# Optimization experiments

Measured on AMD Instinct MI355X. Metric: run time of the kernel, lower is better.

The kernel has to match this reference:

```python
import jax, jax.numpy as jnp
import numpy as np

KAPPA = 5  # kNN neighbors per node (module hardcodes kappas = [5]*B, topk of KAPPA+2)


def build_graph(inputs):
    """Vectorized equivalent of get_graph(): returns flat (src, dst, edge_weight)
    over the B*S node space. Filtered kNN edges (dst < 2) are masked via weight 0,
    which is mathematically identical to removing them (gcn_norm uses edge weights)."""
    B, S, _ = inputs.shape
    diff = inputs[:, :, None, :] - inputs[:, None, :, :]            # [B,S,S,2]
    deltas = jnp.sqrt(jnp.sum(diff * diff, axis=-1))                # torch.cdist
    eye = jnp.eye(S, dtype=bool)
    d = jnp.where(eye[None], jnp.inf, deltas)                       # fill_diagonal_(inf)
    nodes = jnp.arange(2, S, dtype=jnp.int32)                       # non-depot nodes
    # depot edges: 0 -> i  and  i -> 1  for i in [2, S)
    src_dep = jnp.concatenate([jnp.zeros(S - 2, jnp.int32), nodes])
    dst_dep = jnp.concatenate([nodes, jnp.ones(S - 2, jnp.int32)])
    # kNN edges: 7 nearest per non-depot node (diag=inf so i never selected)
    _, idx = jax.lax.top_k(-d[:, 2:, :], KAPPA + 2)                 # [B, S-2, 7]
    src_knn = jnp.broadcast_to(nodes[:, None], (S - 2, KAPPA + 2)).reshape(-1)
    dst_knn = idx.reshape(B, -1).astype(jnp.int32)                  # [B, 7*(S-2)]
    mask_knn = (dst_knn >= 2).astype(jnp.float32)                   # drop depot dsts
    src = jnp.concatenate([jnp.broadcast_to(src_dep[None], (B, src_dep.shape[0])), jnp.broadcast_to(src_knn[None], (B, src_knn.shape[0]))], axis=1)
    dst = jnp.concatenate([jnp.broadcast_to(dst_dep[None], (B, dst_dep.shape[0])), dst_knn], axis=1)
    ew = jnp.concatenate([jnp.ones((B, dst_dep.shape[0]), jnp.float32), mask_knn], axis=1)
    offs = (jnp.arange(B, dtype=jnp.int32) * S)[:, None]            # batch node offset
    return (src + offs).reshape(-1), (dst + offs).reshape(-1), ew.reshape(-1)


def gcn_conv(x, src, dst, norm, self_norm, W, b, N):
    h = x @ W                                                       # GCNConv linear
    agg = jax.ops.segment_sum(h[src] * norm[:, None], dst, num_segments=N)
    agg = agg + h * self_norm[:, None]                              # self-loop term
    return agg + b


def gnn_forward(x, src, dst, ew, W0, b0, W1, b1, W2, b2):
    N = x.shape[0]
    deg = jax.ops.segment_sum(ew, dst, num_segments=N) + 1.0        # +1 self-loop
    dinv = 1.0 / jnp.sqrt(deg)
    norm = dinv[src] * dinv[dst] * ew                               # sym gcn_norm
    self_norm = dinv * dinv
    h = jax.nn.relu(gcn_conv(x, src, dst, norm, self_norm, W0, b0, N))
    h = jax.nn.relu(gcn_conv(h, src, dst, norm, self_norm, W1, b1, N))
    return gcn_conv(h, src, dst, norm, self_norm, W2, b2, N)


def setup_inputs() -> dict:
    B, S, D, H = 64, 1000, 128, 512
    key = jax.random.key(0)
    ks = jax.random.split(key, 12)
    sc = lambda fan_in: 1.0 / np.sqrt(fan_in)
    return {
        "inputs": jax.random.uniform(ks[0], (B, S, 2), jnp.float32),
        "scor": jax.random.uniform(ks[1], (B, S, 1), jnp.float32),
        "Wc": jax.random.normal(ks[2], (2, D), jnp.float32) * sc(2),
        "bc": jax.random.normal(ks[3], (D,), jnp.float32) * 0.01,
        "Ws": jax.random.normal(ks[4], (1, D), jnp.float32) * sc(1),
        "bs": jax.random.normal(ks[5], (D,), jnp.float32) * 0.01,
        "W0": jax.random.normal(ks[6], (D, H), jnp.float32) * sc(D),
        "b0": jnp.zeros((H,), jnp.float32),
        "W1": jax.random.normal(ks[8], (H, H), jnp.float32) * sc(H),
        "b1": jnp.zeros((H,), jnp.float32),
        "W2": jax.random.normal(ks[10], (H, D), jnp.float32) * sc(H),
        "b2": jnp.zeros((D,), jnp.float32),
    }


def reference(inputs, scor, Wc, bc, Ws, bs, W0, b0, W1, b1, W2, b2):
    B, S, _ = inputs.shape
    src, dst, ew = build_graph(inputs)
    x = (inputs @ Wc + bc) + (scor @ Ws + bs)                       # embedded_data
    x = x.reshape(B * S, -1)
    out = gnn_forward(x, src, dst, ew, W0, b0, W1, b1, W2, b2)
    return out.reshape(B, S, -1)
```

## Files before the change

### kernel.cpp

```cpp
#include <hip/hip_runtime.h>

typedef unsigned short u16;
typedef unsigned int u32;
typedef unsigned long long u64;
using short8 = __attribute__((ext_vector_type(8))) short;
using f32x4  = __attribute__((ext_vector_type(4))) float;

constexpr int Bb = 64, Ss = 1000, Dd = 128, Hh = 512;
constexpr int NN = Bb * Ss;
constexpr int NSRC = Ss - 2;

__device__ __forceinline__ float bf2f(u16 h) {
    u32 u = ((u32)h) << 16;
    return __builtin_bit_cast(float, u);
}
__device__ __forceinline__ u16 f2bf(float v) {
    u32 u = __builtin_bit_cast(u32, v);
    u32 r = (u + 0x7FFFu + ((u >> 16) & 1u)) >> 16;
    return (u16)r;
}
__device__ __forceinline__ float4 bf4(ushort4 v) {
    float4 r;
    r.x = bf2f(v.x); r.y = bf2f(v.y); r.z = bf2f(v.z); r.w = bf2f(v.w);
    return r;
}
__device__ __forceinline__ void gl_lds16(const void* g, void* l) {
    __builtin_amdgcn_global_load_lds(
        (const __attribute__((address_space(1))) void*)g,
        (__attribute__((address_space(3))) void*)l, 16, 0, 0);
}
__device__ __forceinline__ void acc8(float (&a)[8], uint4 v, float w) {
    u32 c[4] = {v.x, v.y, v.z, v.w};
#pragma unroll
    for (int k = 0; k < 4; ++k) {
        float lo = __builtin_bit_cast(float, c[k] << 16);
        float hi = __builtin_bit_cast(float, c[k] & 0xFFFF0000u);
        a[2 * k]     += lo * w;
        a[2 * k + 1] += hi * w;
    }
}
__device__ __forceinline__ void acc2(float (&a)[2], u32 v, float w) {
    float lo = __builtin_bit_cast(float, v << 16);
    float hi = __builtin_bit_cast(float, v & 0xFFFF0000u);
    a[0] += lo * w;
    a[1] += hi * w;
}
__device__ __forceinline__ void unp8(float (&a)[8], uint4 v) {
    u32 c[4] = {v.x, v.y, v.z, v.w};
#pragma unroll
    for (int k = 0; k < 4; ++k) {
        a[2 * k]     = __builtin_bit_cast(float, c[k] << 16);
        a[2 * k + 1] = __builtin_bit_cast(float, c[k] & 0xFFFF0000u);
    }
}

__device__ __forceinline__ u64 umin64(u64 a, u64 b) { return a < b ? a : b; }
__device__ __forceinline__ u64 umax64(u64 a, u64 b) { return a < b ? b : a; }

__device__ __forceinline__ void ins8u(u64 (&bd)[8], u64 v) {
#pragma unroll
    for (int k = 7; k >= 1; --k)
        bd[k] = umin64(umax64(v, bd[k - 1]), bd[k]);
    bd[0] = umin64(v, bd[0]);
}

__device__ __forceinline__ void merge8(u64 (&a)[8], int mask) {
    u64 b[8];
#pragma unroll
    for (int k = 0; k < 8; ++k)
        b[k] = __shfl_xor((unsigned long long)a[k], mask);
    u64 m[8];
#pragma unroll
    for (int k = 0; k < 8; ++k) m[k] = umin64(a[k], b[7 - k]);
#pragma unroll
    for (int k = 0; k < 4; ++k) {
        u64 lo = umin64(m[k], m[k + 4]), hi = umax64(m[k], m[k + 4]);
        m[k] = lo; m[k + 4] = hi;
    }
#pragma unroll
    for (int base = 0; base < 8; base += 4)
#pragma unroll
        for (int k = 0; k < 2; ++k) {
            u64 lo = umin64(m[base + k], m[base + k + 2]);
            u64 hi = umax64(m[base + k], m[base + k + 2]);
            m[base + k] = lo; m[base + k + 2] = hi;
        }
#pragma unroll
    for (int base = 0; base < 8; base += 2) {
        u64 lo = umin64(m[base], m[base + 1]), hi = umax64(m[base], m[base + 1]);
        m[base] = lo; m[base + 1] = hi;
    }
#pragma unroll
    for (int k = 0; k < 8; ++k) a[k] = m[k];
}

__global__ __launch_bounds__(256) void knn_bin_kernel(const float* __restrict__ inputs,
                                                      float2* __restrict__ gsxy,
                                                      u16* __restrict__ gsid,
                                                      int* __restrict__ gcst) {
    __shared__ float px[Ss], py[Ss];
    __shared__ int hist[256];
    __shared__ int cur[256];
    int b = blockIdx.x;
    int tid = threadIdx.x;
    const float* base = inputs + (size_t)b * Ss * 2;
    for (int t = tid; t < Ss; t += 256) { px[t] = base[2 * t]; py[t] = base[2 * t + 1]; }
    hist[tid] = 0;
    __syncthreads();
    for (int t = tid; t < Ss; t += 256) {
        int cx = min(15, (int)(px[t] * 16.0f));
        int cy = min(15, (int)(py[t] * 16.0f));
        atomicAdd(&hist[cy * 16 + cx], 1);
    }
    __syncthreads();
    int cnt = hist[tid];
    for (int s = 1; s < 256; s <<= 1) {
        int u = (tid >= s) ? hist[tid - s] : 0;
        __syncthreads();
        hist[tid] += u;
        __syncthreads();
    }
    int st = hist[tid] - cnt;
    cur[tid] = st;
    gcst[b * 260 + tid] = st;
    if (tid == 0) gcst[b * 260 + 256] = Ss;
    __syncthreads();
    for (int t = tid; t < Ss; t += 256) {
        float x = px[t], y = py[t];
        int cx = min(15, (int)(x * 16.0f));
        int cy = min(15, (int)(y * 16.0f));
        int p = atomicAdd(&cur[cy * 16 + cx], 1);
        gsxy[b * 1000 + p] = make_float2(x, y);
        gsid[b * 1000 + p] = (u16)t;
    }
}

__global__ __launch_bounds__(256) void knn_query_kernel(const float* __restrict__ inputs,
                                                        const float2* __restrict__ gsxy,
                                                        const u16* __restrict__ gsid,
                                                        const int* __restrict__ gcst,
                                                        u16* __restrict__ knn,
                                                        int* __restrict__ indeg) {
    __shared__ float2 sxy[Ss];
    __shared__ u16 sid[Ss];
    __shared__ int cst[257];
    int b = blockIdx.x;
    int tid = threadIdx.x;
    for (int t = tid; t < Ss; t += 256) { sxy[t] = gsxy[b * 1000 + t]; sid[t] = gsid[b * 1000 + t]; }
    for (int t = tid; t < 257; t += 256) cst[t] = gcst[b * 260 + t];
    __syncthreads();

    int sub = tid & 7;
    int g = tid >> 3;
    int i = 2 + blockIdx.y * 32 + g;
    if (i >= Ss) return;

    float x = inputs[(size_t)b * 2000 + 2 * i];
    float y = inputs[(size_t)b * 2000 + 2 * i + 1];
    int cx = min(15, (int)(x * 16.0f));
    int cy = min(15, (int)(y * 16.0f));
    const float INF = __builtin_inff();
    constexpr float h = 0.0625f;

    u64 bd[8];
    int w = 1;
    for (;;) {
#pragma unroll
        for (int k = 0; k < 8; ++k) bd[k] = ~0ULL;
        int x0 = max(0, cx - w), x1 = min(15, cx + w);
        int y0 = max(0, cy - w), y1 = min(15, cy + w);
        for (int cyy = y0; cyy <= y1; ++cyy) {
            int p0 = cst[cyy * 16 + x0];
            int p1 = cst[cyy * 16 + x1 + 1];
            for (int p = p0 + sub; p < p1; p += 8) {
                float2 q = sxy[p];
                int j = sid[p];
                float dx = __fsub_rn(x, q.x);
                float dy = __fsub_rn(y, q.y);
                float d2 = __fadd_rn(__fmul_rn(dx, dx), __fmul_rn(dy, dy));
                float d = __fsqrt_rn(d2);
                u64 key = (((u64)__builtin_bit_cast(u32, d)) << 32) | (u32)j;
                key = (j == i) ? ~0ULL : key;
                ins8u(bd, key);
            }
        }
        merge8(bd, 1); merge8(bd, 2); merge8(bd, 4);
        float d7 = __builtin_bit_cast(float, (u32)(bd[6] >> 32));
        float bL = (x0 > 0)  ? (x - (float)x0 * h) : INF;
        float bR = (x1 < 15) ? ((float)(x1 + 1) * h - x) : INF;
        float bB = (y0 > 0)  ? (y - (float)y0 * h) : INF;
        float bT = (y1 < 15) ? ((float)(y1 + 1) * h - y) : INF;
        float bound = fminf(fminf(bL, bR), fminf(bB, bT));
        if (d7 <= bound - 2e-6f || w >= 16) break;
        ++w;
    }

    if (sub == 0) {
        u16* kp = knn + ((size_t)b * NSRC + (i - 2)) * 7;
#pragma unroll
        for (int k = 0; k < 7; ++k) {
            int j = (int)(u32)bd[k];
            kp[k] = (u16)j;
            if (j >= 2) atomicAdd(&indeg[b * Ss + j], 1);
        }
    }
}

__global__ __launch_bounds__(1024) void scan1_kernel(const int* __restrict__ indeg,
                                                     int* __restrict__ offs,
                                                     int* __restrict__ bsum,
                                                     float* __restrict__ dinv) {
    __shared__ int sh[1024];
    int t = threadIdx.x;
    int idx = blockIdx.x * 1024 + t;
    int v = (idx < NN) ? indeg[idx] : 0;
    sh[t] = v;
    __syncthreads();
    for (int off = 1; off < 1024; off <<= 1) {
        int u = (t >= off) ? sh[t - off] : 0;
        __syncthreads();
        sh[t] += u;
        __syncthreads();
    }
    if (idx < NN) {
        offs[idx] = sh[t] - v;
        int ii = idx % Ss;
        float deg = (ii == 0) ? 1.0f : (ii == 1) ? (float)(Ss - 1) : (float)(v + 2);
        dinv[idx] = 1.0f / __fsqrt_rn(deg);
    }
    if (t == 1023) bsum[blockIdx.x] = sh[1023];
}

__global__ void scan2_kernel(int* __restrict__ bsum) {
    if (threadIdx.x == 0) {
        int run = 0;
        for (int k = 0; k < 63; ++k) { int v = bsum[k]; bsum[k] = run; run += v; }
        bsum[63] = run;
    }
}

__global__ __launch_bounds__(1024) void scan3_kernel(int* __restrict__ offs,
                                                     const int* __restrict__ bsum) {
    int idx = blockIdx.x * 1024 + threadIdx.x;
    if (idx < NN) offs[idx] += bsum[blockIdx.x];
    if (idx == 0) offs[NN] = bsum[63];
}

__global__ __launch_bounds__(256) void fill_rev_kernel(const u16* __restrict__ knn,
                                                       const int* __restrict__ offs,
                                                       int* __restrict__ cursor,
                                                       u16* __restrict__ rev) {
    if (threadIdx.x >= 250) return;
    int b = blockIdx.x;
    int i = 2 + blockIdx.y * 250 + threadIdx.x;
    if (i >= Ss) return;
    const u16* kp = knn + ((size_t)b * NSRC + (i - 2)) * 7;
#pragma unroll
    for (int k = 0; k < 7; ++k) {
        int d = kp[k];
        if (d >= 2) {
            int n = b * Ss + d;
            int p = atomicAdd(&cursor[n], 1);
            rev[offs[n] + p] = (u16)i;
        }
    }
}

__global__ __launch_bounds__(512) void fuse0_kernel(const float* __restrict__ Wc,
                                                    const float* __restrict__ bc,
                                                    const float* __restrict__ Ws,
                                                    const float* __restrict__ bs,
                                                    const float* __restrict__ W0,
                                                    float* __restrict__ A) {
    int h = threadIdx.x;
    float a0 = 0.f, a1 = 0.f, a2 = 0.f, a3 = 0.f;
    for (int c = 0; c < Dd; ++c) {
        float w = W0[c * Hh + h];
        a0 += Wc[c] * w;
        a1 += Wc[Dd + c] * w;
        a2 += Ws[c] * w;
        a3 += (bc[c] + bs[c]) * w;
    }
    A[h] = a0; A[Hh + h] = a1; A[2 * Hh + h] = a2; A[3 * Hh + h] = a3;
}

__global__ __launch_bounds__(1024) void agg_e_kernel(const float* __restrict__ inputs,
                                                     const float* __restrict__ scor,
                                                     const float* __restrict__ dinv,
                                                     const int* __restrict__ offs,
                                                     const int* __restrict__ indeg,
                                                     const u16* __restrict__ rev,
                                                     float4* __restrict__ ve) {
    __shared__ float se0[Ss], se1[Ss], se2[Ss], sdv[Ss];
    __shared__ float4 depw[16];
    int b = blockIdx.x;
    int tid = threadIdx.x;
    int nb = b * Ss;
    const float* base = inputs + (size_t)nb * 2;
    for (int t = tid; t < Ss; t += 1024) {
        se0[t] = base[2 * t];
        se1[t] = base[2 * t + 1];
        se2[t] = scor[nb + t];
        sdv[t] = dinv[nb + t];
    }
    __syncthreads();

    float4 dep = {0.f, 0.f, 0.f, 0.f};
    for (int r = tid; r < Ss; r += 1024) {
        if (r >= 2) {
            float w = sdv[r];
            dep.x += se0[r] * w; dep.y += se1[r] * w;
            dep.z += se2[r] * w; dep.w += w;
        }
    }
#pragma unroll
    for (int m = 1; m < 64; m <<= 1) {
        dep.x += __shfl_xor(dep.x, m);
        dep.y += __shfl_xor(dep.y, m);
        dep.z += __shfl_xor(dep.z, m);
        dep.w += __shfl_xor(dep.w, m);
    }
    if ((tid & 63) == 0) depw[tid >> 6] = dep;
    __syncthreads();

    int i = tid;
    if (i >= Ss) return;
    float dn = sdv[i], sn = dn * dn;
    float4 acc = {0.f, 0.f, 0.f, 0.f};
    if (i >= 2) {
        int n = nb + i;
        int cnt = indeg[n], o = offs[n];
        float w0 = sdv[0];
        acc.x = se0[0] * w0; acc.y = se1[0] * w0;
        acc.z = se2[0] * w0; acc.w = w0;
        for (int e = 0; e < cnt; ++e) {
            int s = rev[o + e];
            float w = sdv[s];
            acc.x += se0[s] * w; acc.y += se1[s] * w;
            acc.z += se2[s] * w; acc.w += w;
        }
    } else if (i == 1) {
        float4 t = {0.f, 0.f, 0.f, 0.f};
#pragma unroll
        for (int k = 0; k < 16; ++k) {
            t.x += depw[k].x; t.y += depw[k].y;
            t.z += depw[k].z; t.w += depw[k].w;
        }
        acc = t;
    }
    float4 v;
    v.x = acc.x * dn + se0[i] * sn;
    v.y = acc.y * dn + se1[i] * sn;
    v.z = acc.z * dn + se2[i] * sn;
    v.w = acc.w * dn + sn;
    ve[nb + i] = v;
}

__global__ __launch_bounds__(256) void expand512_kernel(const float4* __restrict__ ve,
                                                        const float* __restrict__ A,
                                                        const float* __restrict__ bias,
                                                        u16* __restrict__ X) {
    int gid = blockIdx.x * 256 + threadIdx.x;
    if (gid >= NN * 128) return;
    int n = gid >> 7, t = gid & 127;
    int h = t * 4;
    float4 v = ve[n];
    float4 a0 = *(const float4*)(A + h);
    float4 a1 = *(const float4*)(A + Hh + h);
    float4 a2 = *(const float4*)(A + 2 * Hh + h);
    float4 a3 = *(const float4*)(A + 3 * Hh + h);
    float4 bz = *(const float4*)(bias + h);
    ushort4 o;
    o.x = f2bf(fmaxf(v.x * a0.x + v.y * a1.x + v.z * a2.x + v.w * a3.x + bz.x, 0.f));
    o.y = f2bf(fmaxf(v.x * a0.y + v.y * a1.y + v.z * a2.y + v.w * a3.y + bz.y, 0.f));
    o.z = f2bf(fmaxf(v.x * a0.z + v.y * a1.z + v.z * a2.z + v.w * a3.z + bz.z, 0.f));
    o.w = f2bf(fmaxf(v.x * a0.w + v.y * a1.w + v.z * a2.w + v.w * a3.w + bz.w, 0.f));
    *(ushort4*)(X + (size_t)n * Hh + h) = o;
}

__global__ void transp_kernel(const float* __restrict__ src,
                              u16* __restrict__ dst, int R, int C) {
    int gid = blockIdx.x * 256 + threadIdx.x;
    if (gid >= R * C) return;
    int r = gid / C, c = gid - r * C;
    dst[c * R + r] = f2bf(src[gid]);
}

__global__ __launch_bounds__(256) void gemm_kernel(const u16* __restrict__ A,
                                                   const u16* __restrict__ W,
                                                   u16* __restrict__ Y,
                                                   int K, int Ncols,
                                                   int nyb, int nxb) {
    __shared__ __align__(16) u16 lA[128][64];
    __shared__ __align__(16) u16 lW[128][64];

    int grp = blockIdx.x / (8 * nxb);
    int rem = blockIdx.x - grp * (8 * nxb);
    int xcd = rem & 7;
    int xb  = rem >> 3;
    int yb  = grp * 8 + xcd;
    if (yb >= nyb) return;

    int row0 = yb * 128;
    int col0 = xb * 128;
    int tid = threadIdx.x;
    int lane = tid & 63, wid = tid >> 6;
    int wm = (wid >> 1) * 64, wn = (wid & 1) * 64;
    int lanelo = lane & 15, quad = lane >> 4;

    int lrow = lane >> 3;
    int lslot = lane & 7;

    f32x4 acc[4][4] = {};

    for (int k0 = 0; k0 < K; k0 += 64) {
#pragma unroll
        for (int t = 0; t < 4; ++t) {
            int chunk = t * 4 + wid;
            int row = chunk * 8 + lrow;
            int sc = lslot ^ (row & 7);
            gl_lds16(A + (size_t)(row0 + row) * K + k0 + sc * 8, &lA[chunk * 8][0]);
        }
#pragma unroll
        for (int t = 0; t < 4; ++t) {
            int chunk = t * 4 + wid;
            int row = chunk * 8 + lrow;
            int sc = lslot ^ (row & 7);
            gl_lds16(W + (size_t)(col0 + row) * K + k0 + sc * 8, &lW[chunk * 8][0]);
        }
        __syncthreads();

#pragma unroll
        for (int kk = 0; kk < 64; kk += 32) {
            short8 af[4], bw[4];
            int cbb = (kk >> 3) + quad;
#pragma unroll
            for (int mt = 0; mt < 4; ++mt) {
                int r = wm + mt * 16 + lanelo;
                af[mt] = *(const short8*)&lA[r][((cbb ^ (r & 7))) * 8];
            }
#pragma unroll
            for (int nt = 0; nt < 4; ++nt) {
                int r = wn + nt * 16 + lanelo;
                bw[nt] = *(const short8*)&lW[r][((cbb ^ (r & 7))) * 8];
            }
#pragma unroll
            for (int mt = 0; mt < 4; ++mt)
#pragma unroll
                for (int nt = 0; nt < 4; ++nt)
                    acc[mt][nt] = __builtin_amdgcn_mfma_f32_16x16x32_bf16(
                        af[mt], bw[nt], acc[mt][nt], 0, 0, 0);
        }
        __syncthreads();
    }

#pragma unroll
    for (int mt = 0; mt < 4; ++mt)
#pragma unroll
        for (int nt = 0; nt < 4; ++nt)
#pragma unroll
            for (int r = 0; r < 4; ++r) {
                int row = row0 + wm + mt * 16 + quad * 4 + r;
                int col = col0 + wn + nt * 16 + lanelo;
                Y[(size_t)row * Ncols + col] = f2bf(acc[mt][nt][r]);
            }
}

__global__ __launch_bounds__(1024) void dep1_kernel(const u16* __restrict__ y,
                                                    const float* __restrict__ dinv,
                                                    float* __restrict__ dq,
                                                    int M) {
    int b = blockIdx.x;
    int qq = blockIdx.y;
    int co = blockIdx.z * 128;
    int tid = threadIdx.x;
    int c4 = tid & 31;
    int es = tid >> 5;
    int j0 = 2 + qq * 250;
    int j1 = j0 + 250; if (j1 > Ss) j1 = Ss;
    const u16* yb = y + (size_t)b * Ss * M + co + c4 * 4;
    const float* dv = dinv + b * Ss;
    float a0 = 0.f, a1 = 0.f, a2 = 0.f, a3 = 0.f;
    for (int j = j0 + es; j < j1; j += 32) {
        float w = dv[j];
        float4 u = bf4(*(const ushort4*)(yb + (size_t)j * M));
        a0 += u.x * w; a1 += u.y * w; a2 += u.z * w; a3 += u.w * w;
    }
    __shared__ float4 red[1024];
    float4 mv; mv.x = a0; mv.y = a1; mv.z = a2; mv.w = a3;
    red[tid] = mv;
    __syncthreads();
#pragma unroll
    for (int s = 16; s > 0; s >>= 1) {
        if (es < s) {
            float4 o = red[tid + (s << 5)];
            float4 m = red[tid];
            m.x += o.x; m.y += o.y; m.z += o.z; m.w += o.w;
            red[tid] = m;
        }
        __syncthreads();
    }
    if (es == 0)
        *(float4*)(dq + ((size_t)qq * Bb + b) * M + co + c4 * 4) = red[c4];
}

__global__ __launch_bounds__(256) void aggw512_kernel(const u16* __restrict__ y,
                                                      const float* __restrict__ dinv,
                                                      const int* __restrict__ offs,
                                                      const int* __restrict__ indeg,
                                                      const u16* __restrict__ rev,
                                                      const float* __restrict__ bias,
                                                      const float* __restrict__ dep1,
                                                      u16* __restrict__ oX) {
    int tid = threadIdx.x;
    int wv = tid >> 6, lane = tid & 63;
    int bx = blockIdx.x;
    int b = (bx & 7) + 8 * (bx / 2000);
    int i = ((bx >> 3) % 250) * 4 + wv;
    int nb = b * Ss;
    int n = nb + i;
    const u16* yB = y + (size_t)nb * 512 + lane * 8;

    float acc[8] = {};
    if (i >= 2) {
        int cnt = indeg[n], o = offs[n];
        int rv = 0; float rw = 0.f;
        if (lane < 16 && lane < cnt) { rv = rev[o + lane]; rw = dinv[nb + rv]; }
        float w0 = dinv[nb];
        uint4 v0 = *(const uint4*)yB;
        acc8(acc, v0, w0);
        int cl = cnt < 16 ? cnt : 16;
        int e = 0;
        for (; e + 4 <= cl; e += 4) {
            int   s0 = __shfl(rv, e),     s1 = __shfl(rv, e + 1);
            int   s2 = __shfl(rv, e + 2), s3 = __shfl(rv, e + 3);
            float w_0 = __shfl(rw, e),     w_1 = __shfl(rw, e + 1);
            float w_2 = __shfl(rw, e + 2), w_3 = __shfl(rw, e + 3);
            uint4 u0 = *(const uint4*)(yB + (size_t)s0 * 512);
            uint4 u1 = *(const uint4*)(yB + (size_t)s1 * 512);
            uint4 u2 = *(const uint4*)(yB + (size_t)s2 * 512);
            uint4 u3 = *(const uint4*)(yB + (size_t)s3 * 512);
            acc8(acc, u0, w_0); acc8(acc, u1, w_1);
            acc8(acc, u2, w_2); acc8(acc, u3, w_3);
        }
        for (; e < cl; ++e) {
            int s = __shfl(rv, e); float ww = __shfl(rw, e);
            uint4 u = *(const uint4*)(yB + (size_t)s * 512);
            acc8(acc, u, ww);
        }
        for (; e < cnt; ++e) {
            int s = rev[o + e]; float ww = dinv[nb + s];
            uint4 u = *(const uint4*)(yB + (size_t)s * 512);
            acc8(acc, u, ww);
        }
    } else if (i == 1) {
        const float* dp = dep1 + (size_t)b * 512 + lane * 8;
#pragma unroll
        for (int qq = 0; qq < 4; ++qq) {
            float4 v0 = *(const float4*)(dp + (size_t)qq * Bb * 512);
            float4 v1 = *(const float4*)(dp + (size_t)qq * Bb * 512 + 4);
            acc[0] += v0.x; acc[1] += v0.y; acc[2] += v0.z; acc[3] += v0.w;
            acc[4] += v1.x; acc[5] += v1.y; acc[6] += v1.z; acc[7] += v1.w;
        }
    }
    float dn = dinv[n], sn = dn * dn;
    float s8[8];
    unp8(s8, *(const uint4*)(yB + (size_t)i * 512));
    float4 bl = *(const float4*)(bias + lane * 8);
    float4 bh = *(const float4*)(bias + lane * 8 + 4);
    float bz[8] = {bl.x, bl.y, bl.z, bl.w, bh.x, bh.y, bh.z, bh.w};
    u32 ow[4];
#pragma unroll
    for (int k = 0; k < 4; ++k) {
        float z0 = acc[2 * k]     * dn + s8[2 * k]     * sn + bz[2 * k];
        float z1 = acc[2 * k + 1] * dn + s8[2 * k + 1] * sn + bz[2 * k + 1];
        ow[k] = (u32)f2bf(fmaxf(z0, 0.f)) | ((u32)f2bf(fmaxf(z1, 0.f)) << 16);
    }
    uint4 ov = {ow[0], ow[1], ow[2], ow[3]};
    *(uint4*)(oX + (size_t)n * 512 + lane * 8) = ov;
}

__global__ __launch_bounds__(256) void aggwf128_kernel(const u16* __restrict__ y,
                                                       const float* __restrict__ dinv,
                                                       const int* __restrict__ offs,
                                                       const int* __restrict__ indeg,
                                                       const u16* __restrict__ rev,
                                                       const float* __restrict__ bias,
                                                       const float* __restrict__ dep1,
                                                       float* __restrict__ out) {
    int tid = threadIdx.x;
    int wv = tid >> 6, lane = tid & 63;
    int bx = blockIdx.x;
    int b = (bx & 7) + 8 * (bx / 2000);
    int i = ((bx >> 3) % 250) * 4 + wv;
    int nb = b * Ss;
    int n = nb + i;
    const u16* yB = y + (size_t)nb * 128 + lane * 2;

    float acc[2] = {};
    if (i >= 2) {
        int cnt = indeg[n], o = offs[n];
        int rv = 0; float rw = 0.f;
        if (lane < 16 && lane < cnt) { rv = rev[o + lane]; rw = dinv[nb + rv]; }
        float w0 = dinv[nb];
        acc2(acc, *(const u32*)yB, w0);
        int cl = cnt < 16 ? cnt : 16;
        int e = 0;
        for (; e + 4 <= cl; e += 4) {
            int   s0 = __shfl(rv, e),     s1 = __shfl(rv, e + 1);
            int   s2 = __shfl(rv, e + 2), s3 = __shfl(rv, e + 3);
            float w_0 = __shfl(rw, e),     w_1 = __shfl(rw, e + 1);
            float w_2 = __shfl(rw, e + 2), w_3 = __shfl(rw, e + 3);
            u32 u0 = *(const u32*)(yB + (size_t)s0 * 128);
            u32 u1 = *(const u32*)(yB + (size_t)s1 * 128);
            u32 u2 = *(const u32*)(yB + (size_t)s2 * 128);
            u32 u3 = *(const u32*)(yB + (size_t)s3 * 128);
            acc2(acc, u0, w_0); acc2(acc, u1, w_1);
            acc2(acc, u2, w_2); acc2(acc, u3, w_3);
        }
        for (; e < cl; ++e) {
            int s = __shfl(rv, e); float ww = __shfl(rw, e);
            acc2(acc, *(const u32*)(yB + (size_t)s * 128), ww);
        }
        for (; e < cnt; ++e) {
            int s = rev[o + e]; float ww = dinv[nb + s];
            acc2(acc, *(const u32*)(yB + (size_t)s * 128), ww);
        }
    } else if (i == 1) {
        const float* dp = dep1 + (size_t)b * 128 + lane * 2;
#pragma unroll
        for (int qq = 0; qq < 4; ++qq) {
            float2 v = *(const float2*)(dp + (size_t)qq * Bb * 128);
            acc[0] += v.x; acc[1] += v.y;
        }
    }
    float dn = dinv[n], sn = dn * dn;
    u32 sv = *(const u32*)(yB + (size_t)i * 128);
    float s0 = __builtin_bit_cast(float, sv << 16);
    float s1 = __builtin_bit_cast(float, sv & 0xFFFF0000u);
    float2 bz = *(const float2*)(bias + lane * 2);
    float2 z;
    z.x = acc[0] * dn + s0 * sn + bz.x;
    z.y = acc[1] * dn + s1 * sn + bz.y;
    *(float2*)(out + (size_t)n * 128 + lane * 2) = z;
}

constexpr size_t O_INDEG  = 0;
constexpr size_t O_CURSOR = 256000;
constexpr size_t O_OFFS   = 512000;
constexpr size_t O_DINV   = 768256;
constexpr size_t O_KNN    = 1024256;
constexpr size_t O_REV    = 1918080;
constexpr size_t O_AMAT   = 2811904;
constexpr size_t O_WT1    = 2942976;
constexpr size_t O_WT2    = 3467264;
constexpr size_t O_X      = 3598336;
constexpr size_t O_Y      = 69134336;
constexpr size_t O_DEP1A  = 134670336;
constexpr size_t O_DEP1B  = 135194624;
constexpr size_t O_BSUM   = 135325696;
constexpr size_t O_GSXY   = O_X;
constexpr size_t O_GSID   = O_X + 512000;
constexpr size_t O_GCST   = O_X + 640000;
constexpr size_t O_VE     = O_Y;

extern "C" void kernel_launch(void* const* d_in, const int* in_sizes, int n_in,
                              void* d_out, int out_size, void* d_ws, size_t ws_size,
                              hipStream_t stream) {
    const float* inputs = (const float*)d_in[0];
    const float* scor   = (const float*)d_in[1];
    const float* Wc     = (const float*)d_in[2];
    const float* bc     = (const float*)d_in[3];
    const float* Ws     = (const float*)d_in[4];
    const float* bs     = (const float*)d_in[5];
    const float* W0     = (const float*)d_in[6];
    const float* b0     = (const float*)d_in[7];
    const float* W1     = (const float*)d_in[8];
    const float* b1     = (const float*)d_in[9];
    const float* W2     = (const float*)d_in[10];
    const float* b2     = (const float*)d_in[11];

    char* w = (char*)d_ws;
    int*    indeg  = (int*)(w + O_INDEG);
    int*    cursor = (int*)(w + O_CURSOR);
    int*    offs   = (int*)(w + O_OFFS);
    float*  dinv   = (float*)(w + O_DINV);
    u16*    knn    = (u16*)(w + O_KNN);
    u16*    rev    = (u16*)(w + O_REV);
    float*  amat   = (float*)(w + O_AMAT);
    u16*    wt1    = (u16*)(w + O_WT1);
    u16*    wt2    = (u16*)(w + O_WT2);
    u16*    xbf    = (u16*)(w + O_X);
    u16*    ybf    = (u16*)(w + O_Y);
    float*  dep1a  = (float*)(w + O_DEP1A);
    float*  dep1b  = (float*)(w + O_DEP1B);
    int*    bsum   = (int*)(w + O_BSUM);
    float2* gsxy   = (float2*)(w + O_GSXY);
    u16*    gsid   = (u16*)(w + O_GSID);
    int*    gcst   = (int*)(w + O_GCST);
    float4* ve     = (float4*)(w + O_VE);

    hipMemsetAsync(w + O_INDEG, 0, 512000, stream);

    knn_bin_kernel<<<Bb, 256, 0, stream>>>(inputs, gsxy, gsid, gcst);
    knn_query_kernel<<<dim3(Bb, 32), 256, 0, stream>>>(inputs, gsxy, gsid, gcst, knn, indeg);
    scan1_kernel<<<63, 1024, 0, stream>>>(indeg, offs, bsum, dinv);
    scan2_kernel<<<1, 64, 0, stream>>>(bsum);
    scan3_kernel<<<63, 1024, 0, stream>>>(offs, bsum);
    fill_rev_kernel<<<dim3(Bb, 4), 256, 0, stream>>>(knn, offs, cursor, rev);

    fuse0_kernel<<<1, 512, 0, stream>>>(Wc, bc, Ws, bs, W0, amat);
    transp_kernel<<<(Hh * Hh + 255) / 256, 256, 0, stream>>>(W1, wt1, Hh, Hh);
    transp_kernel<<<(Hh * Dd + 255) / 256, 256, 0, stream>>>(W2, wt2, Hh, Dd);

    agg_e_kernel<<<Bb, 1024, 0, stream>>>(inputs, scor, dinv, offs, indeg, rev, ve);
    expand512_kernel<<<NN * 128 / 256, 256, 0, stream>>>(ve, amat, b0, xbf);
    gemm_kernel<<<63 * 32, 256, 0, stream>>>(xbf, wt1, ybf, Hh, Hh, 500, 4);
    dep1_kernel<<<dim3(Bb, 4, 4), 1024, 0, stream>>>(ybf, dinv, dep1a, Hh);
    aggw512_kernel<<<NN / 4, 256, 0, stream>>>(ybf, dinv, offs, indeg, rev, b1, dep1a, xbf);
    gemm_kernel<<<63 * 8, 256, 0, stream>>>(xbf, wt2, ybf, Hh, Dd, 500, 1);
    dep1_kernel<<<dim3(Bb, 4, 1), 1024, 0, stream>>>(ybf, dinv, dep1b, Dd);
    aggwf128_kernel<<<NN / 4, 256, 0, stream>>>(ybf, dinv, offs, indeg, rev, b2, dep1b, (float*)d_out);
}
```

Baseline: 321.0 us.

## Fuse depot-1 reduction into aggregation kernels via block-level atomics

Removes the separate dep1 reduction kernels. Each aggregation block now accumulates the dinv-weighted rows of its nodes into shared memory and atomically adds them into a per-batch depot accumulator. Small finalize kernels then compute node 1's output. This avoids a second full read of y, at the cost of float atomics, whose summation order is nondeterministic, and extra tiny launches plus a memset.

```diff
diff --git a/kernel.cpp b/kernel.cpp
--- a/kernel.cpp
+++ b/kernel.cpp
@@ -466,52 +466,15 @@
             }
 }
 
-__global__ __launch_bounds__(1024) void dep1_kernel(const u16* __restrict__ y,
-                                                    const float* __restrict__ dinv,
-                                                    float* __restrict__ dq,
-                                                    int M) {
-    int b = blockIdx.x;
-    int qq = blockIdx.y;
-    int co = blockIdx.z * 128;
-    int tid = threadIdx.x;
-    int c4 = tid & 31;
-    int es = tid >> 5;
-    int j0 = 2 + qq * 250;
-    int j1 = j0 + 250; if (j1 > Ss) j1 = Ss;
-    const u16* yb = y + (size_t)b * Ss * M + co + c4 * 4;
-    const float* dv = dinv + b * Ss;
-    float a0 = 0.f, a1 = 0.f, a2 = 0.f, a3 = 0.f;
-    for (int j = j0 + es; j < j1; j += 32) {
-        float w = dv[j];
-        float4 u = bf4(*(const ushort4*)(yb + (size_t)j * M));
-        a0 += u.x * w; a1 += u.y * w; a2 += u.z * w; a3 += u.w * w;
-    }
-    __shared__ float4 red[1024];
-    float4 mv; mv.x = a0; mv.y = a1; mv.z = a2; mv.w = a3;
-    red[tid] = mv;
-    __syncthreads();
-#pragma unroll
-    for (int s = 16; s > 0; s >>= 1) {
-        if (es < s) {
-            float4 o = red[tid + (s << 5)];
-            float4 m = red[tid];
-            m.x += o.x; m.y += o.y; m.z += o.z; m.w += o.w;
-            red[tid] = m;
-        }
-        __syncthreads();
-    }
-    if (es == 0)
-        *(float4*)(dq + ((size_t)qq * Bb + b) * M + co + c4 * 4) = red[c4];
-}
-
 __global__ __launch_bounds__(256) void aggw512_kernel(const u16* __restrict__ y,
                                                       const float* __restrict__ dinv,
                                                       const int* __restrict__ offs,
                                                       const int* __restrict__ indeg,
                                                       const u16* __restrict__ rev,
                                                       const float* __restrict__ bias,
-                                                      const float* __restrict__ dep1,
+                                                      float* __restrict__ dep,
                                                       u16* __restrict__ oX) {
+    __shared__ float reds[4][512];
     int tid = threadIdx.x;
     int wv = tid >> 6, lane = tid & 63;
     int bx = blockIdx.x;
@@ -521,6 +484,7 @@
     int n = nb + i;
     const u16* yB = y + (size_t)nb * 512 + lane * 8;
 
+    uint4 sv = *(const uint4*)(yB + (size_t)i * 512);
     float acc[8] = {};
     if (i >= 2) {
         int cnt = indeg[n], o = offs[n];
@@ -553,19 +517,14 @@
             uint4 u = *(const uint4*)(yB + (size_t)s * 512);
             acc8(acc, u, ww);
         }
-    } else if (i == 1) {
-        const float* dp = dep1 + (size_t)b * 512 + lane * 8;
-#pragma unroll
-        for (int qq = 0; qq < 4; ++qq) {
-            float4 v0 = *(const float4*)(dp + (size_t)qq * Bb * 512);
-            float4 v1 = *(const float4*)(dp + (size_t)qq * Bb * 512 + 4);
-            acc[0] += v0.x; acc[1] += v0.y; acc[2] += v0.z; acc[3] += v0.w;
-            acc[4] += v1.x; acc[5] += v1.y; acc[6] += v1.z; acc[7] += v1.w;
-        }
     }
     float dn = dinv[n], sn = dn * dn;
     float s8[8];
-    unp8(s8, *(const uint4*)(yB + (size_t)i * 512));
+    unp8(s8, sv);
+    float wdep = (i >= 2) ? dn : 0.f;
+#pragma unroll
+    for (int k = 0; k < 8; ++k) reds[wv][lane * 8 + k] = s8[k] * wdep;
+
     float4 bl = *(const float4*)(bias + lane * 8);
     float4 bh = *(const float4*)(bias + lane * 8 + 4);
     float bz[8] = {bl.x, bl.y, bl.z, bl.w, bh.x, bh.y, bh.z, bh.w};
@@ -574,6 +533,41 @@
     for (int k = 0; k < 4; ++k) {
         float z0 = acc[2 * k]     * dn + s8[2 * k]     * sn + bz[2 * k];
         float z1 = acc[2 * k + 1] * dn + s8[2 * k + 1] * sn + bz[2 * k + 1];
+        ow[k] = (u32)f2bf(fmaxf(z0, 0.f)) | ((u32)f2bf(fmaxf(z1, 0.f)) << 16);
+    }
+    uint4 ov = {ow[0], ow[1], ow[2], ow[3]};
+    *(uint4*)(oX + (size_t)n * 512 + lane * 8) = ov;
+
+    __syncthreads();
+    if (wv == 0) {
+#pragma unroll
+        for (int k = 0; k < 8; ++k) {
+            int c = lane * 8 + k;
+            float s = (reds[0][c] + reds[1][c]) + (reds[2][c] + reds[3][c]);
+            atomicAdd(&dep[b * 512 + c], s);
+        }
+    }
+}
+
+__global__ __launch_bounds__(64) void fin512_kernel(const u16* __restrict__ y,
+                                                    const float* __restrict__ dinv,
+                                                    const float* __restrict__ dep,
+                                                    const float* __restrict__ bias,
+                                                    u16* __restrict__ oX) {
+    int b = blockIdx.x, lane = threadIdx.x;
+    int n = b * Ss + 1;
+    float dn = dinv[n], sn = dn * dn;
+    float s8[8];
+    unp8(s8, *(const uint4*)(y + (size_t)n * 512 + lane * 8));
+    const float* dp = dep + b * 512 + lane * 8;
+    float4 bl = *(const float4*)(bias + lane * 8);
+    float4 bh = *(const float4*)(bias + lane * 8 + 4);
+    float bz[8] = {bl.x, bl.y, bl.z, bl.w, bh.x, bh.y, bh.z, bh.w};
+    u32 ow[4];
+#pragma unroll
+    for (int k = 0; k < 4; ++k) {
+        float z0 = dp[2 * k]     * dn + s8[2 * k]     * sn + bz[2 * k];
+        float z1 = dp[2 * k + 1] * dn + s8[2 * k + 1] * sn + bz[2 * k + 1];
         ow[k] = (u32)f2bf(fmaxf(z0, 0.f)) | ((u32)f2bf(fmaxf(z1, 0.f)) << 16);
     }
     uint4 ov = {ow[0], ow[1], ow[2], ow[3]};
@@ -586,8 +580,9 @@
                                                        const int* __restrict__ indeg,
                                                        const u16* __restrict__ rev,
                                                        const float* __restrict__ bias,
-                                                       const float* __restrict__ dep1,
+                                                       float* __restrict__ dep,
                                                        float* __restrict__ out) {
+    __shared__ float reds[4][128];
     int tid = threadIdx.x;
     int wv = tid >> 6, lane = tid & 63;
     int bx = blockIdx.x;
@@ -597,6 +592,7 @@
     int n = nb + i;
     const u16* yB = y + (size_t)nb * 128 + lane * 2;
 
+    u32 sv = *(const u32*)(yB + (size_t)i * 128);
     float acc[2] = {};
     if (i >= 2) {
         int cnt = indeg[n], o = offs[n];
@@ -626,22 +622,47 @@
             int s = rev[o + e]; float ww = dinv[nb + s];
             acc2(acc, *(const u32*)(yB + (size_t)s * 128), ww);
         }
-    } else if (i == 1) {
-        const float* dp = dep1 + (size_t)b * 128 + lane * 2;
-#pragma unroll
-        for (int qq = 0; qq < 4; ++qq) {
-            float2 v = *(const float2*)(dp + (size_t)qq * Bb * 128);
-            acc[0] += v.x; acc[1] += v.y;
-        }
     }
     float dn = dinv[n], sn = dn * dn;
-    u32 sv = *(const u32*)(yB + (size_t)i * 128);
     float s0 = __builtin_bit_cast(float, sv << 16);
     float s1 = __builtin_bit_cast(float, sv & 0xFFFF0000u);
+    float wdep = (i >= 2) ? dn : 0.f;
+    reds[wv][lane * 2]     = s0 * wdep;
+    reds[wv][lane * 2 + 1] = s1 * wdep;
+
     float2 bz = *(const float2*)(bias + lane * 2);
     float2 z;
     z.x = acc[0] * dn + s0 * sn + bz.x;
     z.y = acc[1] * dn + s1 * sn + bz.y;
+    *(float2*)(out + (size_t)n * 128 + lane * 2) = z;
+
+    __syncthreads();
+    if (wv == 0) {
+#pragma unroll
+        for (int k = 0; k < 2; ++k) {
+            int c = lane * 2 + k;
+            float s = (reds[0][c] + reds[1][c]) + (reds[2][c] + reds[3][c]);
+            atomicAdd(&dep[b * 128 + c], s);
+        }
+    }
+}
+
+__global__ __launch_bounds__(64) void fin128_kernel(const u16* __restrict__ y,
+                                                    const float* __restrict__ dinv,
+                                                    const float* __restrict__ dep,
+                                                    const float* __restrict__ bias,
+                                                    float* __restrict__ out) {
+    int b = blockIdx.x, lane = threadIdx.x;
+    int n = b * Ss + 1;
+    float dn = dinv[n], sn = dn * dn;
+    u32 sv = *(const u32*)(y + (size_t)n * 128 + lane * 2);
+    float s0 = __builtin_bit_cast(float, sv << 16);
+    float s1 = __builtin_bit_cast(float, sv & 0xFFFF0000u);
+    const float* dp = dep + b * 128 + lane * 2;
+    float2 bz = *(const float2*)(bias + lane * 2);
+    float2 z;
+    z.x = dp[0] * dn + s0 * sn + bz.x;
+    z.y = dp[1] * dn + s1 * sn + bz.y;
     *(float2*)(out + (size_t)n * 128 + lane * 2) = z;
 }
 
@@ -657,7 +678,7 @@
 constexpr size_t O_X      = 3598336;
 constexpr size_t O_Y      = 69134336;
 constexpr size_t O_DEP1A  = 134670336;
-constexpr size_t O_DEP1B  = 135194624;
+constexpr size_t O_DEP1B  = 134801408;
 constexpr size_t O_BSUM   = 135325696;
 constexpr size_t O_GSXY   = O_X;
 constexpr size_t O_GSID   = O_X + 512000;
@@ -701,6 +722,7 @@
     float4* ve     = (float4*)(w + O_VE);
 
     hipMemsetAsync(w + O_INDEG, 0, 512000, stream);
+    hipMemsetAsync(w + O_DEP1A, 0, 131072 + 32768, stream);
 
     knn_bin_kernel<<<Bb, 256, 0, stream>>>(inputs, gsxy, gsid, gcst);
     knn_query_kernel<<<dim3(Bb, 32), 256, 0, stream>>>(inputs, gsxy, gsid, gcst, knn, indeg);
@@ -716,9 +738,9 @@
     agg_e_kernel<<<Bb, 1024, 0, stream>>>(inputs, scor, dinv, offs, indeg, rev, ve);
     expand512_kernel<<<NN * 128 / 256, 256, 0, stream>>>(ve, amat, b0, xbf);
     gemm_kernel<<<63 * 32, 256, 0, stream>>>(xbf, wt1, ybf, Hh, Hh, 500, 4);
-    dep1_kernel<<<dim3(Bb, 4, 4), 1024, 0, stream>>>(ybf, dinv, dep1a, Hh);
     aggw512_kernel<<<NN / 4, 256, 0, stream>>>(ybf, dinv, offs, indeg, rev, b1, dep1a, xbf);
+    fin512_kernel<<<Bb, 64, 0, stream>>>(ybf, dinv, dep1a, b1, xbf);
     gemm_kernel<<<63 * 8, 256, 0, stream>>>(xbf, wt2, ybf, Hh, Dd, 500, 1);
-    dep1_kernel<<<dim3(Bb, 4, 1), 1024, 0, stream>>>(ybf, dinv, dep1b, Dd);
     aggwf128_kernel<<<NN / 4, 256, 0, stream>>>(ybf, dinv, offs, indeg, rev, b2, dep1b, (float*)d_out);
-}
+    fin128_kernel<<<Bb, 64, 0, stream>>>(ybf, dinv, dep1b, b2, (float*)d_out);
+}
```

Result: slower. 786.2 us (+144.9%).

## Compute depot-1 aggregate from layer input sums instead of reading GEMM output

Applied to the files above, without the earlier changes.

The layer-1 depot aggregation (node 1 sums dinv-weighted features of all non-depot nodes) is now computed as (sum of dinv*x) @ W1, using linearity. The per-batch weighted sum is accumulated inside the expand kernel while it writes X, and a small fp32 kernel multiplies it by W1. This removes the dep1 pass that re-read the full 512-wide GEMM output. The result now comes from an fp32 matmul rather than summing bf16-rounded GEMM outputs, which changes rounding slightly. The expand kernel also becomes a looped, shared-memory-staged launch with fewer blocks.

```diff
diff --git a/kernel.cpp b/kernel.cpp
--- a/kernel.cpp
+++ b/kernel.cpp
@@ -356,26 +356,94 @@
     ve[nb + i] = v;
 }
 
-__global__ __launch_bounds__(256) void expand512_kernel(const float4* __restrict__ ve,
-                                                        const float* __restrict__ A,
-                                                        const float* __restrict__ bias,
-                                                        u16* __restrict__ X) {
-    int gid = blockIdx.x * 256 + threadIdx.x;
-    if (gid >= NN * 128) return;
-    int n = gid >> 7, t = gid & 127;
-    int h = t * 4;
-    float4 v = ve[n];
-    float4 a0 = *(const float4*)(A + h);
-    float4 a1 = *(const float4*)(A + Hh + h);
-    float4 a2 = *(const float4*)(A + 2 * Hh + h);
-    float4 a3 = *(const float4*)(A + 3 * Hh + h);
-    float4 bz = *(const float4*)(bias + h);
-    ushort4 o;
-    o.x = f2bf(fmaxf(v.x * a0.x + v.y * a1.x + v.z * a2.x + v.w * a3.x + bz.x, 0.f));
-    o.y = f2bf(fmaxf(v.x * a0.y + v.y * a1.y + v.z * a2.y + v.w * a3.y + bz.y, 0.f));
-    o.z = f2bf(fmaxf(v.x * a0.z + v.y * a1.z + v.z * a2.z + v.w * a3.z + bz.z, 0.f));
-    o.w = f2bf(fmaxf(v.x * a0.w + v.y * a1.w + v.z * a2.w + v.w * a3.w + bz.w, 0.f));
-    *(ushort4*)(X + (size_t)n * Hh + h) = o;
+__global__ __launch_bounds__(256) void expand512p_kernel(const float4* __restrict__ ve,
+                                                         const float* __restrict__ dinv,
+                                                         const float* __restrict__ A,
+                                                         const float* __restrict__ bias,
+                                                         u16* __restrict__ X,
+                                                         float* __restrict__ sxp) {
+    __shared__ float4 sve[250];
+    __shared__ float  sdv[250];
+    __shared__ float  sred[8][256];
+    int bx = blockIdx.x;
+    int g = bx >> 1, cg = bx & 1;
+    int b = blockIdx.y;
+    int n0 = g * 250;
+    int nb = b * Ss;
+    int tid = threadIdx.x;
+    int c32 = tid & 31, slice = tid >> 5;
+    int ch = cg * 256 + c32 * 8;
+    for (int t = tid; t < 250; t += 256) {
+        sve[t] = ve[nb + n0 + t];
+        sdv[t] = dinv[nb + n0 + t];
+    }
+    __syncthreads();
+
+    float A0[8], A1[8], A2[8], A3[8], BZ[8];
+#pragma unroll
+    for (int j = 0; j < 8; ++j) {
+        A0[j] = A[ch + j];
+        A1[j] = A[Hh + ch + j];
+        A2[j] = A[2 * Hh + ch + j];
+        A3[j] = A[3 * Hh + ch + j];
+        BZ[j] = bias[ch + j];
+    }
+    float acc[8] = {};
+    for (int t = slice; t < 250; t += 8) {
+        int n = n0 + t;
+        float4 v = sve[t];
+        float dw = (n >= 2) ? sdv[t] : 0.f;
+        u32 ow[4];
+#pragma unroll
+        for (int j = 0; j < 4; ++j) {
+            float z0 = fmaxf(v.x * A0[2 * j]     + v.y * A1[2 * j]     + v.z * A2[2 * j]     + v.w * A3[2 * j]     + BZ[2 * j],     0.f);
+            float z1 = fmaxf(v.x * A0[2 * j + 1] + v.y * A1[2 * j + 1] + v.z * A2[2 * j + 1] + v.w * A3[2 * j + 1] + BZ[2 * j + 1], 0.f);
+            u16 h0 = f2bf(z0), h1 = f2bf(z1);
+            ow[j] = (u32)h0 | ((u32)h1 << 16);
+            acc[2 * j]     += dw * bf2f(h0);
+            acc[2 * j + 1] += dw * bf2f(h1);
+        }
+        uint4 o = {ow[0], ow[1], ow[2], ow[3]};
+        *(uint4*)(X + (size_t)(nb + n) * Hh + ch) = o;
+    }
+#pragma unroll
+    for (int j = 0; j < 8; ++j) sred[slice][c32 * 8 + j] = acc[j];
+    __syncthreads();
+    if (slice == 0) {
+#pragma unroll
+        for (int j = 0; j < 8; ++j) {
+            float s = 0.f;
+#pragma unroll
+            for (int sl = 0; sl < 8; ++sl) s += sred[sl][c32 * 8 + j];
+            sxp[((size_t)b * 4 + g) * Hh + ch + j] = s;
+        }
+    }
+}
+
+__global__ __launch_bounds__(512) void sxw1_kernel(const float* __restrict__ sxp,
+                                                   const float* __restrict__ W1,
+                                                   float* __restrict__ depf) {
+    __shared__ float sx8[8][512];
+    int bb0 = blockIdx.x * 8;
+    int tid = threadIdx.x;
+    for (int idx = tid; idx < 8 * 512; idx += 512) {
+        int bi = idx >> 9, k = idx & 511;
+        float s = 0.f;
+#pragma unroll
+        for (int g = 0; g < 4; ++g)
+            s += sxp[((size_t)(bb0 + bi) * 4 + g) * 512 + k];
+        sx8[bi][k] = s;
+    }
+    __syncthreads();
+    float a[8] = {};
+    for (int k = 0; k < 512; ++k) {
+        float wv = W1[(size_t)k * 512 + tid];
+#pragma unroll
+        for (int bi = 0; bi < 8; ++bi) a[bi] += sx8[bi][k] * wv;
+    }
+#pragma unroll
+    for (int bi = 0; bi < 8; ++bi)
+        depf[(size_t)(bb0 + bi) * 512 + tid] = a[bi];
 }
 
 __global__ void transp_kernel(const float* __restrict__ src,
@@ -555,13 +623,10 @@
         }
     } else if (i == 1) {
         const float* dp = dep1 + (size_t)b * 512 + lane * 8;
-#pragma unroll
-        for (int qq = 0; qq < 4; ++qq) {
-            float4 v0 = *(const float4*)(dp + (size_t)qq * Bb * 512);
-            float4 v1 = *(const float4*)(dp + (size_t)qq * Bb * 512 + 4);
-            acc[0] += v0.x; acc[1] += v0.y; acc[2] += v0.z; acc[3] += v0.w;
-            acc[4] += v1.x; acc[5] += v1.y; acc[6] += v1.z; acc[7] += v1.w;
-        }
+        float4 v0 = *(const float4*)dp;
+        float4 v1 = *(const float4*)(dp + 4);
+        acc[0] = v0.x; acc[1] = v0.y; acc[2] = v0.z; acc[3] = v0.w;
+        acc[4] = v1.x; acc[5] = v1.y; acc[6] = v1.z; acc[7] = v1.w;
     }
     float dn = dinv[n], sn = dn * dn;
     float s8[8];
@@ -656,8 +721,8 @@
 constexpr size_t O_WT2    = 3467264;
 constexpr size_t O_X      = 3598336;
 constexpr size_t O_Y      = 69134336;
-constexpr size_t O_DEP1A  = 134670336;
-constexpr size_t O_DEP1B  = 135194624;
+constexpr size_t O_SXP    = 134670336;
+constexpr size_t O_DEPF   = 135194624;
 constexpr size_t O_BSUM   = 135325696;
 constexpr size_t O_GSXY   = O_X;
 constexpr size_t O_GSID   = O_X + 512000;
@@ -692,8 +757,8 @@
     u16*    wt2    = (u16*)(w + O_WT2);
     u16*    xbf    = (u16*)(w + O_X);
     u16*    ybf    = (u16*)(w + O_Y);
-    float*  dep1a  = (float*)(w + O_DEP1A);
-    float*  dep1b  = (float*)(w + O_DEP1B);
+    float*  sxp    = (float*)(w + O_SXP);
+    float*  depf   = (float*)(w + O_DEPF);
     int*    bsum   = (int*)(w + O_BSUM);
     float2* gsxy   = (float2*)(w + O_GSXY);
     u16*    gsid   = (u16*)(w + O_GSID);
@@ -714,11 +779,11 @@
     transp_kernel<<<(Hh * Dd + 255) / 256, 256, 0, stream>>>(W2, wt2, Hh, Dd);
 
     agg_e_kernel<<<Bb, 1024, 0, stream>>>(inputs, scor, dinv, offs, indeg, rev, ve);
-    expand512_kernel<<<NN * 128 / 256, 256, 0, stream>>>(ve, amat, b0, xbf);
+    expand512p_kernel<<<dim3(8, Bb), 256, 0, stream>>>(ve, dinv, amat, b0, xbf, sxp);
+    sxw1_kernel<<<8, 512, 0, stream>>>(sxp, W1, depf);
     gemm_kernel<<<63 * 32, 256, 0, stream>>>(xbf, wt1, ybf, Hh, Hh, 500, 4);
-    dep1_kernel<<<dim3(Bb, 4, 4), 1024, 0, stream>>>(ybf, dinv, dep1a, Hh);
-    aggw512_kernel<<<NN / 4, 256, 0, stream>>>(ybf, dinv, offs, indeg, rev, b1, dep1a, xbf);
+    aggw512_kernel<<<NN / 4, 256, 0, stream>>>(ybf, dinv, offs, indeg, rev, b1, depf, xbf);
     gemm_kernel<<<63 * 8, 256, 0, stream>>>(xbf, wt2, ybf, Hh, Dd, 500, 1);
-    dep1_kernel<<<dim3(Bb, 4, 1), 1024, 0, stream>>>(ybf, dinv, dep1b, Dd);
-    aggwf128_kernel<<<NN / 4, 256, 0, stream>>>(ybf, dinv, offs, indeg, rev, b2, dep1b, (float*)d_out);
-}
+    dep1_kernel<<<dim3(Bb, 4, 1), 1024, 0, stream>>>(ybf, dinv, depf, Dd);
+    aggwf128_kernel<<<NN / 4, 256, 0, stream>>>(ybf, dinv, offs, indeg, rev, b2, depf, (float*)d_out);
+}
```

Measured after the change: 357.9 us. 11.5% more time.
